# Kernel optimization log

Hardware: AMD Instinct MI355X
Metric: run time of the kernel (lower is better)

The kernel has to match this reference:

```python
import jax, jax.numpy as jnp
import numpy as np

EMBED_DIM = 1024
NUM_HEADS = 16
HEAD_DIM = EMBED_DIM // NUM_HEADS
SCALING = HEAD_DIM ** -0.5
NEG_FILL = -1e30


def setup_inputs() -> dict:
    key = jax.random.key(0)
    k1, k2, k3 = jax.random.split(key, 3)
    T, B, E = 2048, 4, EMBED_DIM
    query = jax.random.normal(k1, (T, B, E), dtype=jnp.float32)
    key_padding_mask = jnp.zeros((B, T), dtype=bool)  # 1 = padded key
    # xavier_uniform-like init
    lim_in = (6.0 / (3 * E + E)) ** 0.5
    in_proj_weight = jax.random.uniform(k2, (3 * E, E), minval=-lim_in, maxval=lim_in, dtype=jnp.float32)
    in_proj_bias = jnp.zeros((3 * E,), dtype=jnp.float32)
    lim_out = (6.0 / (E + E)) ** 0.5
    out_w = jax.random.uniform(k3, (E, E), minval=-lim_out, maxval=lim_out, dtype=jnp.float32)
    out_b = jnp.zeros((E,), dtype=jnp.float32)
    return {"query": query, "key_padding_mask": key_padding_mask,
            "in_proj_weight": in_proj_weight, "in_proj_bias": in_proj_bias,
            "out_w": out_w, "out_b": out_b}


def reference(query, key_padding_mask, in_proj_weight, in_proj_bias, out_w, out_b):
    T, B, E = query.shape
    H, D = NUM_HEADS, HEAD_DIM
    # fused in-projection (self-attention: qkv from same input)
    qkv = query @ in_proj_weight.T + in_proj_bias  # [T,B,3E]
    q, k, v = jnp.split(qkv, 3, axis=-1)
    q = q * SCALING
    q = q.reshape(T, B, H, D)
    k = k.reshape(T, B, H, D)
    v = v.reshape(T, B, H, D)
    # attention scores [B,H,T,S]
    scores = jnp.einsum('tbhd,sbhd->bhts', q, k)
    scores = jnp.where(key_padding_mask[:, None, None, :], NEG_FILL, scores)
    attn_w = jax.nn.softmax(scores, axis=-1)  # [B,H,T,S]
    # weighted sum of values -> [T,B,E]
    attn = jnp.einsum('bhts,sbhd->tbhd', attn_w, v).reshape(T, B, E)
    attn = attn @ out_w.T + out_b
    attn_w_avg = jnp.sum(attn_w, axis=1) / H  # [B,T,S]
    return attn, attn_w_avg
```

## Files before the change

### kernel.cpp

```cpp
#include <hip/hip_runtime.h>
#include <stdint.h>

#define QSCALE 0.18033688011112042f

typedef unsigned short u16;
typedef unsigned int u32;
typedef unsigned long long u64;
typedef _Float16 f16;
typedef __attribute__((ext_vector_type(2))) __fp16 h16x2;
typedef __attribute__((ext_vector_type(8))) _Float16 f16x8;
typedef __attribute__((ext_vector_type(8))) __bf16 bf16x8;
typedef __attribute__((ext_vector_type(4))) float f32x4;
typedef __attribute__((ext_vector_type(16))) float f32x16;
typedef __attribute__((ext_vector_type(8))) u16 u16x8;
typedef __attribute__((ext_vector_type(4))) u32 u32x4;

__device__ __forceinline__ void gl_lds16(const void* g, void* l) {
  __builtin_amdgcn_global_load_lds(
      (const __attribute__((address_space(1))) void*)g,
      (__attribute__((address_space(3))) void*)l, 16, 0, 0);
}

__device__ __forceinline__ u16 f2bf(float f) {
  unsigned int u = __float_as_uint(f);
  u += 0x7FFFu + ((u >> 16) & 1u);
  return (u16)(u >> 16);
}

extern "C" __global__ __launch_bounds__(256) void cvt_all(
    const float* __restrict__ query, const float* __restrict__ w_in,
    const float* __restrict__ w_out, u16* __restrict__ dst,
    const unsigned char* __restrict__ mask, u64* __restrict__ mbits) {
  if (blockIdx.x == 12288) {
    const int i = threadIdx.x;
    if (i < 128) {
      const unsigned char* p = mask + i * 64;
      u64 bits = 0;
#pragma unroll
      for (int j = 0; j < 8; ++j) {
        const u64 c = *(const u64*)(p + j * 8);
#pragma unroll
        for (int bb = 0; bb < 8; ++bb)
          if ((c >> (8 * bb)) & 0xFFull) bits |= 1ull << (j * 8 + bb);
      }
      mbits[i] = bits;
    }
    return;
  }
  int i = (blockIdx.x * 256 + threadIdx.x) * 4;
  const float* src;
  int off;
  if (i < 8388608) {
    src = query; off = i;
  } else if (i < 11534336) {
    src = w_in; off = i - 8388608;
  } else {
    src = w_out; off = i - 11534336;
  }
  float4 v = *(const float4*)(src + off);
  ushort4 o;
  o.x = f2bf(v.x); o.y = f2bf(v.y); o.z = f2bf(v.z); o.w = f2bf(v.w);
  *(ushort4*)(dst + i) = o;
}

extern "C" __global__ __launch_bounds__(256) void gemm_qkv(
    const u16* __restrict__ X, const u16* __restrict__ W,
    const float* __restrict__ bias,
    u16* __restrict__ qb, u16* __restrict__ kb, u16* __restrict__ vtb) {
  const int tid = threadIdx.x;
  const int w = tid >> 6, lane = tid & 63;
  const int lg = lane >> 4, ll = lane & 15;
  const int wm = w >> 1, wn = w & 1;

  const int xcd = blockIdx.x & 7;
  const int i6 = blockIdx.x >> 3;
  const int tx = xcd * 8 + (i6 & 7);
  const int ty = i6 >> 3;
  const int row0A = tx * 128;
  const int row0B = ty * 128;

  __shared__ __align__(16) u16 SM[16384];
  u16* Asb = SM;
  u16* Bsb = SM + 8192;

  f32x4 acc[4][4] = {};

  const int r_st = tid >> 2;
  const int cb_st = (tid & 3) * 16;

#pragma unroll
  for (int it = 0; it < 2; ++it) {
    gl_lds16((const char*)X + ((size_t)(row0A + it * 64 + r_st) * 1024) * 2 + cb_st,
             (char*)Asb + it * 4096 + w * 1024);
    gl_lds16((const char*)W + ((size_t)(row0B + it * 64 + r_st) * 1024) * 2 + cb_st,
             (char*)Bsb + it * 4096 + w * 1024);
  }

  for (int kt = 0; kt < 32; ++kt) {
    const int cur = kt & 1;
    asm volatile("s_waitcnt vmcnt(0)" ::: "memory");
    __syncthreads();
    if (kt + 1 < 32) {
      const int k0 = (kt + 1) * 32;
      const int nxt = cur ^ 1;
#pragma unroll
      for (int it = 0; it < 2; ++it) {
        gl_lds16((const char*)X + ((size_t)(row0A + it * 64 + r_st) * 1024 + k0) * 2 + cb_st,
                 (char*)(Asb + nxt * 4096) + it * 4096 + w * 1024);
        gl_lds16((const char*)W + ((size_t)(row0B + it * 64 + r_st) * 1024 + k0) * 2 + cb_st,
                 (char*)(Bsb + nxt * 4096) + it * 4096 + w * 1024);
      }
    }
    const u16* Ab = Asb + cur * 4096;
    const u16* Bb = Bsb + cur * 4096;
    const int kc = lg * 8;
    bf16x8 a[4], bfr[4];
#pragma unroll
    for (int i = 0; i < 4; ++i)
      a[i] = *(const bf16x8*)(Ab + (wm * 64 + i * 16 + ll) * 32 + kc);
#pragma unroll
    for (int j = 0; j < 4; ++j)
      bfr[j] = *(const bf16x8*)(Bb + (wn * 64 + j * 16 + ll) * 32 + kc);
#pragma unroll
    for (int i = 0; i < 4; ++i)
#pragma unroll
      for (int j = 0; j < 4; ++j)
        acc[i][j] = __builtin_amdgcn_mfma_f32_16x16x32_bf16(a[i], bfr[j], acc[i][j], 0, 0, 0);
  }

  __syncthreads();
  const int which = row0B >> 10;
  const float scl = which == 0 ? QSCALE : 1.0f;
  const int hh0 = (row0B & 1023) >> 6;

#pragma unroll
  for (int j = 0; j < 4; ++j) {
    const int n = row0B + wn * 64 + j * 16 + ll;
    const float bv = bias[n];
#pragma unroll
    for (int i = 0; i < 4; ++i)
#pragma unroll
      for (int r = 0; r < 4; ++r) {
        const float val = (acc[i][j][r] + bv) * scl;
        u16 pay;
        if (which == 2) {
          const f16 hv = (f16)val;
          pay = __builtin_bit_cast(u16, hv);
        } else {
          pay = f2bf(val);
        }
        const int lrow = wn * 128 + r * 32 + wm * 16 + i * 4 + lg;
        const int slot = (j * 2 + (ll >> 3)) ^ (lrow & 7);
        SM[lrow * 64 + slot * 8 + (ll & 7)] = pay;
      }
  }
  __syncthreads();

  if (which < 2) {
    u16* dst = which ? kb : qb;
    const int lrow = tid;
    const int hh = hh0 + (lrow >> 7);
    const int bb = (lrow >> 5) & 3;
    const int tt = (row0A >> 2) + (lrow & 31);
    u16* gp = dst + ((size_t)(bb * 16 + hh) * 2048 + tt) * 64;
#pragma unroll
    for (int s = 0; s < 8; ++s)
      *(u16x8*)(gp + s * 8) = *(const u16x8*)(SM + lrow * 64 + ((s ^ (lrow & 7)) << 3));
  } else {
#pragma unroll
    for (int u = 0; u < 2; ++u) {
      const int rid = u * 256 + tid;
      const int bb = rid >> 7, hhr = (rid >> 6) & 1, dd = rid & 63;
      const int hh = hh0 + hhr;
      const int slot0 = dd >> 3, de = dd & 7;
      u16 col[32];
#pragma unroll
      for (int t2 = 0; t2 < 32; ++t2) {
        const int lrow = hhr * 128 + bb * 32 + t2;
        col[t2] = SM[lrow * 64 + ((slot0 ^ (lrow & 7)) << 3) + de];
      }
      u16* gp = vtb + ((size_t)(bb * 16 + hh) * 64 + dd) * 2048 + (row0A >> 2);
#pragma unroll
      for (int sg = 0; sg < 4; ++sg)
        *(u16x8*)(gp + sg * 8) = *(const u16x8*)(col + sg * 8);
    }
  }
}

extern "C" __global__ __launch_bounds__(256, 4) void flash_fwd(
    const u16* __restrict__ q, const u16* __restrict__ k,
    const u16* __restrict__ vt, const u64* __restrict__ mbits,
    u16* __restrict__ attn_pre, float* __restrict__ stat_il) {
  const int lb = ((blockIdx.x & 7) << 7) + (blockIdx.x >> 3);
  const int bh = lb >> 4, tt = lb & 15;
  const int b = bh >> 4, hd = bh & 15;
  const int t0 = tt * 128;
  const int tid = threadIdx.x, w = tid >> 6, lane = tid & 63;
  const int hl = lane >> 5;
  const int l31 = lane & 31;

  __shared__ __align__(16) u16 Ks[2][64 * 64];
  __shared__ __align__(16) u16 Vs[2][64 * 64];

  const int qrow = t0 + w * 32 + l31;
  const u16* qp = q + ((size_t)bh * 2048 + qrow) * 64 + hl * 8;
  bf16x8 qreg[4];
#pragma unroll
  for (int kg = 0; kg < 4; ++kg) qreg[kg] = *(const bf16x8*)(qp + kg * 16);

  f32x16 po[2] = {};
  float ls0 = 0.f, ls1 = 0.f;
  const h16x2 ones = {(__fp16)1.0f, (__fp16)1.0f};

  const int slot_r = tid >> 3;
  const int slot_c8 = (tid & 7) ^ (slot_r & 7);

#define STAGE_F(buf, s0_)                                                      \
  do {                                                                         \
    _Pragma("unroll") for (int it2 = 0; it2 < 2; ++it2) {                      \
      const int rr = it2 * 32 + slot_r;                                        \
      gl_lds16((const char*)k +                                                \
                   (((size_t)bh * 2048 + (s0_) + rr) * 64 + slot_c8 * 8) * 2,  \
               (char*)&Ks[buf][0] + it2 * 4096 + w * 1024);                    \
      gl_lds16((const char*)vt +                                               \
                   (((size_t)bh * 64 + rr) * 2048 + (s0_) + slot_c8 * 8) * 2,  \
               (char*)&Vs[buf][0] + it2 * 4096 + w * 1024);                    \
    }                                                                          \
  } while (0)

  STAGE_F(0, 0);
  asm volatile("s_waitcnt vmcnt(0)" ::: "memory");
  __builtin_amdgcn_s_barrier();

  for (int t = 0; t < 32; ++t) {
    const u64 mb = mbits[b * 32 + t];
    const int cur = t & 1;
    if (t + 1 < 32) STAGE_F(cur ^ 1, (t + 1) * 64);

    const char* Kb = (const char*)&Ks[cur][0];
    const char* Vb = (const char*)&Vs[cur][0];

#pragma unroll
    for (int kt = 0; kt < 2; ++kt) {
      f32x16 z = {};
      const int key = kt * 32 + l31;
      __builtin_amdgcn_s_setprio(1);
#pragma unroll
      for (int kg = 0; kg < 4; ++kg) {
        const bf16x8 kf = *(const bf16x8*)(
            Kb + key * 128 + ((((kg << 1) | hl) ^ (key & 7)) << 4));
        z = __builtin_amdgcn_mfma_f32_32x32x16_bf16(kf, qreg[kg], z, 0, 0, 0);
      }
      __builtin_amdgcn_s_setprio(0);

      float ps[16];
#pragma unroll
      for (int r = 0; r < 16; ++r) ps[r] = __builtin_amdgcn_exp2f(z[r]);
      const u32 m32 = (u32)(mb >> (kt * 32));
      if (m32) {
#pragma unroll
        for (int r = 0; r < 16; ++r) {
          const int bitpos = (r & 3) + 8 * (r >> 2) + 4 * hl;
          if ((m32 >> bitpos) & 1u) ps[r] = 0.f;
        }
      }

      u32 w8[8];
#pragma unroll
      for (int j = 0; j < 8; ++j) {
        const h16x2 pk = __builtin_amdgcn_cvt_pkrtz(ps[2 * j], ps[2 * j + 1]);
        w8[j] = __builtin_bit_cast(u32, pk);
        if (j & 1)
          ls1 = __builtin_amdgcn_fdot2(pk, ones, ls1, false);
        else
          ls0 = __builtin_amdgcn_fdot2(pk, ones, ls0, false);
      }

#pragma unroll
      for (int f = 0; f < 2; ++f) {
        u32 d0 = w8[4 * f], d1 = w8[4 * f + 1];
        u32 s0w = w8[4 * f + 2], s1w = w8[4 * f + 3];
        asm volatile("v_permlane32_swap_b32 %0, %1" : "+v"(d0), "+v"(s0w));
        asm volatile("v_permlane32_swap_b32 %0, %1" : "+v"(d1), "+v"(s1w));
        const f16x8 pa = __builtin_bit_cast(f16x8, (u32x4){d0, d1, s0w, s1w});
        const int g = kt * 2 + f;
        __builtin_amdgcn_s_setprio(1);
#pragma unroll
        for (int dt = 0; dt < 2; ++dt) {
          const int d = dt * 32 + l31;
          const f16x8 vf = *(const f16x8*)(
              Vb + d * 128 + ((((g << 1) | hl) ^ (d & 7)) << 4));
          po[dt] = __builtin_amdgcn_mfma_f32_32x32x16_f16(pa, vf, po[dt], 0, 0, 0);
        }
        __builtin_amdgcn_s_setprio(0);
      }
    }

    asm volatile("s_waitcnt vmcnt(0)" ::: "memory");
    __builtin_amdgcn_s_barrier();
  }

  float lsum = ls0 + ls1;
  lsum += __shfl_xor(lsum, 32, 64);
  const float linv = 1.0f / lsum;
  if (lane < 32)
    stat_il[(size_t)bh * 2048 + t0 + w * 32 + lane] = linv;

#pragma unroll
  for (int r = 0; r < 16; ++r) {
    const int qi = (r & 3) + 8 * (r >> 2) + 4 * hl;
    const float lv = __shfl(linv, qi, 64);
    const int trow = t0 + w * 32 + qi;
#pragma unroll
    for (int dt = 0; dt < 2; ++dt) {
      const int dd = dt * 32 + l31;
      attn_pre[((size_t)(trow * 4 + b)) * 1024 + hd * 64 + dd] =
          f2bf(po[dt][r] * lv);
    }
  }
#undef STAGE_F
}

extern "C" __global__ __launch_bounds__(256, 3) void tail_fused(
    const u16* __restrict__ q, const u16* __restrict__ k,
    const u64* __restrict__ mbits, const float* __restrict__ stat_il,
    float* __restrict__ wout,
    const u16* __restrict__ A, const u16* __restrict__ Wo,
    const float* __restrict__ bias, float* __restrict__ out) {
  __shared__ __align__(16) u16 POOL[24576];
  const int bid = blockIdx.x;
  const int g5 = bid / 5, r5 = bid % 5;
  const int tid = threadIdx.x, w = tid >> 6, lane = tid & 63;

  if (r5 == 4) {
    const int lg = lane >> 4, ll = lane & 15;
    const int wm = w >> 1, wn = w & 1;
    const int xcd = g5 & 7;
    const int i6 = g5 >> 3;
    const int row0A = (xcd * 8 + (i6 & 7)) * 128;
    const int row0B = (i6 >> 3) * 128;

    u16* Asb = POOL;
    u16* Bsb = POOL + 8192;

    f32x4 acc[4][4] = {};
    const int r_st = tid >> 2;
    const int cb_st = (tid & 3) * 16;

#pragma unroll
    for (int it = 0; it < 2; ++it) {
      gl_lds16((const char*)A + ((size_t)(row0A + it * 64 + r_st) * 1024) * 2 + cb_st,
               (char*)Asb + it * 4096 + w * 1024);
      gl_lds16((const char*)Wo + ((size_t)(row0B + it * 64 + r_st) * 1024) * 2 + cb_st,
               (char*)Bsb + it * 4096 + w * 1024);
    }

    for (int kt = 0; kt < 32; ++kt) {
      const int cur = kt & 1;
      asm volatile("s_waitcnt vmcnt(0)" ::: "memory");
      __syncthreads();
      if (kt + 1 < 32) {
        const int k0 = (kt + 1) * 32;
        const int nxt = cur ^ 1;
#pragma unroll
        for (int it = 0; it < 2; ++it) {
          gl_lds16((const char*)A + ((size_t)(row0A + it * 64 + r_st) * 1024 + k0) * 2 + cb_st,
                   (char*)(Asb + nxt * 4096) + it * 4096 + w * 1024);
          gl_lds16((const char*)Wo + ((size_t)(row0B + it * 64 + r_st) * 1024 + k0) * 2 + cb_st,
                   (char*)(Bsb + nxt * 4096) + it * 4096 + w * 1024);
        }
      }
      const u16* Ab = Asb + cur * 4096;
      const u16* Bb = Bsb + cur * 4096;
      const int kc = lg * 8;
      bf16x8 a[4], bfr[4];
#pragma unroll
      for (int i = 0; i < 4; ++i)
        a[i] = *(const bf16x8*)(Ab + (wm * 64 + i * 16 + ll) * 32 + kc);
#pragma unroll
      for (int j = 0; j < 4; ++j)
        bfr[j] = *(const bf16x8*)(Bb + (wn * 64 + j * 16 + ll) * 32 + kc);
#pragma unroll
      for (int i = 0; i < 4; ++i)
#pragma unroll
        for (int j = 0; j < 4; ++j)
          acc[i][j] = __builtin_amdgcn_mfma_f32_16x16x32_bf16(a[i], bfr[j], acc[i][j], 0, 0, 0);
    }

#pragma unroll
    for (int j = 0; j < 4; ++j) {
      const int n = row0B + wn * 64 + j * 16 + ll;
      const float bv = bias[n];
#pragma unroll
      for (int i = 0; i < 4; ++i)
#pragma unroll
        for (int r = 0; r < 4; ++r) {
          const int m = row0A + wm * 64 + i * 16 + lg * 4 + r;
          out[(size_t)m * 1024 + n] = acc[i][j][r] + bv;
        }
    }
    return;
  }

  const int wb = g5 * 4 + r5;
  const int lb = ((wb & 7) << 8) + (wb >> 3);
  const int b = lb >> 9, tt = (lb >> 5) & 15, st = lb & 31;
  const int t0 = tt * 128, s0 = st * 64;
  const int hl = lane >> 5;
  const int l31 = lane & 31;

  const int slot_r8 = tid >> 3;
  const int slot_c8 = (tid & 7) ^ (slot_r8 & 7);

  const u64 mbw = mbits[b * 32 + st];
  const u32 m32lo = (u32)mbw, m32hi = (u32)(mbw >> 32);
  const bool domask = mbw != 0ull;

#define STAGE_W(buf, hh)                                                       \
  do {                                                                         \
    const size_t qo_ = (size_t)(b * 16 + (hh)) * 2048;                         \
    _Pragma("unroll") for (int i2 = 0; i2 < 4; ++i2) {                         \
      const int rr = i2 * 32 + slot_r8;                                        \
      gl_lds16((const char*)q + ((qo_ + t0 + rr) * 64 + slot_c8 * 8) * 2,      \
               (char*)(POOL + (buf)*8192) + i2 * 4096 + w * 1024);             \
    }                                                                          \
    _Pragma("unroll") for (int i2 = 0; i2 < 2; ++i2) {                         \
      const int rr = i2 * 32 + slot_r8;                                        \
      gl_lds16((const char*)k + ((qo_ + s0 + rr) * 64 + slot_c8 * 8) * 2,      \
               (char*)(POOL + 16384 + (buf)*4096) + i2 * 4096 + w * 1024);     \
    }                                                                          \
  } while (0)

  STAGE_W(0, 0);
  asm volatile("s_waitcnt vmcnt(0)" ::: "memory");
  __syncthreads();

  float accw[32] = {};
  for (int h = 0; h < 16; ++h) {
    const int cur = h & 1;
    const float ilh =
        stat_il[(size_t)(b * 16 + h) * 2048 + t0 + w * 32 + l31];

    if (h + 1 < 16) STAGE_W(cur ^ 1, h + 1);

    const char* Qb = (const char*)(POOL + cur * 8192);
    const char* Kb = (const char*)(POOL + 16384 + cur * 4096);

    const int qr = w * 32 + l31;
    bf16x8 qf[4];
#pragma unroll
    for (int kg = 0; kg < 4; ++kg)
      qf[kg] = *(const bf16x8*)(
          Qb + qr * 128 + ((((kg << 1) | hl) ^ (qr & 7)) << 4));

    f32x16 z0 = {}, z1 = {};
    __builtin_amdgcn_s_setprio(1);
#pragma unroll
    for (int kg = 0; kg < 4; ++kg) {
      const int key = l31;
      const bf16x8 kf = *(const bf16x8*)(
          Kb + key * 128 + ((((kg << 1) | hl) ^ (key & 7)) << 4));
      z0 = __builtin_amdgcn_mfma_f32_32x32x16_bf16(kf, qf[kg], z0, 0, 0, 0);
    }
#pragma unroll
    for (int kg = 0; kg < 4; ++kg) {
      const int key = 32 + l31;
      const bf16x8 kf = *(const bf16x8*)(
          Kb + key * 128 + ((((kg << 1) | hl) ^ (key & 7)) << 4));
      z1 = __builtin_amdgcn_mfma_f32_32x32x16_bf16(kf, qf[kg], z1, 0, 0, 0);
    }
    __builtin_amdgcn_s_setprio(0);

#pragma unroll
    for (int r = 0; r < 16; ++r) {
      float p = __builtin_amdgcn_exp2f(z0[r]);
      if (domask) {
        const int bitpos = (r & 3) + 8 * (r >> 2) + 4 * hl;
        if ((m32lo >> bitpos) & 1u) p = 0.f;
      }
      accw[r] = fmaf(p, ilh, accw[r]);
    }
#pragma unroll
    for (int r = 0; r < 16; ++r) {
      float p = __builtin_amdgcn_exp2f(z1[r]);
      if (domask) {
        const int bitpos = (r & 3) + 8 * (r >> 2) + 4 * hl;
        if ((m32hi >> bitpos) & 1u) p = 0.f;
      }
      accw[16 + r] = fmaf(p, ilh, accw[16 + r]);
    }

    asm volatile("s_waitcnt vmcnt(0)" ::: "memory");
    __syncthreads();
  }

  float* tb = ((float*)POOL) + w * 2048;
#pragma unroll
  for (int kt = 0; kt < 2; ++kt)
#pragma unroll
    for (int j = 0; j < 4; ++j) {
      f32x4 qd;
#pragma unroll
      for (int e = 0; e < 4; ++e) qd[e] = accw[kt * 16 + 4 * j + e] * 0.0625f;
      const int slot = kt * 8 + 2 * j + hl;
      *(f32x4*)(tb + l31 * 64 + ((slot ^ (l31 & 7)) << 2)) = qd;
    }
  __syncthreads();
#pragma unroll
  for (int j2 = 0; j2 < 8; ++j2) {
    const int row = j2 * 4 + (lane >> 4);
    const int slot = lane & 15;
    const f32x4 v = *(const f32x4*)(tb + row * 64 + ((slot ^ (row & 7)) << 2));
    *(f32x4*)(wout + ((size_t)b * 2048 + t0 + w * 32 + row) * 2048 + s0 +
              slot * 4) = v;
  }
#undef STAGE_W
}

extern "C" void kernel_launch(void* const* d_in, const int* in_sizes, int n_in,
                              void* d_out, int out_size, void* d_ws, size_t ws_size,
                              hipStream_t stream) {
  const float* query = (const float*)d_in[0];
  const unsigned char* mask = (const unsigned char*)d_in[1];
  const float* w_in = (const float*)d_in[2];
  const float* b_in = (const float*)d_in[3];
  const float* w_out = (const float*)d_in[4];
  const float* b_out = (const float*)d_in[5];

  float* out0 = (float*)d_out;
  float* outw = out0 + (size_t)8388608;

  char* ws = (char*)d_ws;
  u16* Xbf   = (u16*)(ws + 0);
  u16* Wqkv  = (u16*)(ws + 16777216);
  u16* Woutb = (u16*)(ws + 23068672);
  u16* qb    = (u16*)(ws + 25165824);
  u16* kb    = (u16*)(ws + 41943040);
  u16* vtb   = (u16*)(ws + 75497472);
  u16* ap    = (u16*)(ws + 92274688);
  float* sil = (float*)(ws + 109051904);
  u64* mbits = (u64*)(ws + 109576192);

  cvt_all<<<12289, 256, 0, stream>>>(query, w_in, w_out, Xbf, mask, mbits);
  gemm_qkv<<<1536, 256, 0, stream>>>(Xbf, Wqkv, b_in, qb, kb, vtb);
  flash_fwd<<<1024, 256, 0, stream>>>(qb, kb, vtb, mbits, ap, sil);
  tail_fused<<<2560, 256, 0, stream>>>(qb, kb, mbits, sil, outw,
                                       ap, Woutb, b_out, out0);
}
```

Baseline: 269.5 us.

## Widen attention-weight tiles to 128 keys per block in tail kernel

The tail kernel's attention-weight blocks now cover 128 key columns instead of 64, so each Q tile staged per head is reused across twice as many keys. That halves Q loads and block count. The grid shrinks from 2560 to 1536 blocks, still interleaving one out-projection GEMM block for every two weight blocks. LDS grows to 64 KB and the accumulator doubles to 64 floats, so occupancy is lowered to 2 blocks per SM. The output write-back is rewritten so each thread stores half of a 128-wide row.

```diff
diff --git a/kernel.cpp b/kernel.cpp
--- a/kernel.cpp
+++ b/kernel.cpp
@@ -321,22 +321,22 @@
 #undef STAGE_F
 }
 
-extern "C" __global__ __launch_bounds__(256, 3) void tail_fused(
+extern "C" __global__ __launch_bounds__(256, 2) void tail_fused(
     const u16* __restrict__ q, const u16* __restrict__ k,
     const u64* __restrict__ mbits, const float* __restrict__ stat_il,
     float* __restrict__ wout,
     const u16* __restrict__ A, const u16* __restrict__ Wo,
     const float* __restrict__ bias, float* __restrict__ out) {
-  __shared__ __align__(16) u16 POOL[24576];
+  __shared__ __align__(16) u16 POOL[32768];
   const int bid = blockIdx.x;
-  const int g5 = bid / 5, r5 = bid % 5;
+  const int g3 = bid / 3, r3 = bid % 3;
   const int tid = threadIdx.x, w = tid >> 6, lane = tid & 63;
 
-  if (r5 == 4) {
+  if (r3 == 2) {
     const int lg = lane >> 4, ll = lane & 15;
     const int wm = w >> 1, wn = w & 1;
-    const int xcd = g5 & 7;
-    const int i6 = g5 >> 3;
+    const int xcd = g3 & 7;
+    const int i6 = g3 >> 3;
     const int row0A = (xcd * 8 + (i6 & 7)) * 128;
     const int row0B = (i6 >> 3) * 128;
 
@@ -402,19 +402,24 @@
     return;
   }
 
-  const int wb = g5 * 4 + r5;
-  const int lb = ((wb & 7) << 8) + (wb >> 3);
-  const int b = lb >> 9, tt = (lb >> 5) & 15, st = lb & 31;
-  const int t0 = tt * 128, s0 = st * 64;
+  const int wb = g3 * 2 + r3;
+  const int lb = ((wb & 7) << 7) + (wb >> 3);
+  const int b = lb >> 8, tt = (lb >> 4) & 15, sp = lb & 15;
+  const int t0 = tt * 128, s0 = sp * 128;
   const int hl = lane >> 5;
   const int l31 = lane & 31;
 
   const int slot_r8 = tid >> 3;
   const int slot_c8 = (tid & 7) ^ (slot_r8 & 7);
 
-  const u64 mbw = mbits[b * 32 + st];
-  const u32 m32lo = (u32)mbw, m32hi = (u32)(mbw >> 32);
-  const bool domask = mbw != 0ull;
+  u32 m32t[4];
+  {
+    const u64 mb0 = mbits[b * 32 + sp * 2];
+    const u64 mb1 = mbits[b * 32 + sp * 2 + 1];
+    m32t[0] = (u32)mb0; m32t[1] = (u32)(mb0 >> 32);
+    m32t[2] = (u32)mb1; m32t[3] = (u32)(mb1 >> 32);
+  }
+  const bool domask = (m32t[0] | m32t[1] | m32t[2] | m32t[3]) != 0u;
 
 #define STAGE_W(buf, hh)                                                       \
   do {                                                                         \
@@ -423,11 +428,8 @@
       const int rr = i2 * 32 + slot_r8;                                        \
       gl_lds16((const char*)q + ((qo_ + t0 + rr) * 64 + slot_c8 * 8) * 2,      \
                (char*)(POOL + (buf)*8192) + i2 * 4096 + w * 1024);             \
-    }                                                                          \
-    _Pragma("unroll") for (int i2 = 0; i2 < 2; ++i2) {                         \
-      const int rr = i2 * 32 + slot_r8;                                        \
       gl_lds16((const char*)k + ((qo_ + s0 + rr) * 64 + slot_c8 * 8) * 2,      \
-               (char*)(POOL + 16384 + (buf)*4096) + i2 * 4096 + w * 1024);     \
+               (char*)(POOL + 16384 + (buf)*8192) + i2 * 4096 + w * 1024);     \
     }                                                                          \
   } while (0)
 
@@ -435,7 +437,7 @@
   asm volatile("s_waitcnt vmcnt(0)" ::: "memory");
   __syncthreads();
 
-  float accw[32] = {};
+  float accw[64] = {};
   for (int h = 0; h < 16; ++h) {
     const int cur = h & 1;
     const float ilh =
@@ -444,7 +446,7 @@
     if (h + 1 < 16) STAGE_W(cur ^ 1, h + 1);
 
     const char* Qb = (const char*)(POOL + cur * 8192);
-    const char* Kb = (const char*)(POOL + 16384 + cur * 4096);
+    const char* Kb = (const char*)(POOL + 16384 + cur * 8192);
 
     const int qr = w * 32 + l31;
     bf16x8 qf[4];
@@ -453,66 +455,55 @@
       qf[kg] = *(const bf16x8*)(
           Qb + qr * 128 + ((((kg << 1) | hl) ^ (qr & 7)) << 4));
 
-    f32x16 z0 = {}, z1 = {};
-    __builtin_amdgcn_s_setprio(1);
-#pragma unroll
-    for (int kg = 0; kg < 4; ++kg) {
-      const int key = l31;
-      const bf16x8 kf = *(const bf16x8*)(
-          Kb + key * 128 + ((((kg << 1) | hl) ^ (key & 7)) << 4));
-      z0 = __builtin_amdgcn_mfma_f32_32x32x16_bf16(kf, qf[kg], z0, 0, 0, 0);
-    }
-#pragma unroll
-    for (int kg = 0; kg < 4; ++kg) {
-      const int key = 32 + l31;
-      const bf16x8 kf = *(const bf16x8*)(
-          Kb + key * 128 + ((((kg << 1) | hl) ^ (key & 7)) << 4));
-      z1 = __builtin_amdgcn_mfma_f32_32x32x16_bf16(kf, qf[kg], z1, 0, 0, 0);
-    }
-    __builtin_amdgcn_s_setprio(0);
-
-#pragma unroll
-    for (int r = 0; r < 16; ++r) {
-      float p = __builtin_amdgcn_exp2f(z0[r]);
-      if (domask) {
-        const int bitpos = (r & 3) + 8 * (r >> 2) + 4 * hl;
-        if ((m32lo >> bitpos) & 1u) p = 0.f;
-      }
-      accw[r] = fmaf(p, ilh, accw[r]);
-    }
-#pragma unroll
-    for (int r = 0; r < 16; ++r) {
-      float p = __builtin_amdgcn_exp2f(z1[r]);
-      if (domask) {
-        const int bitpos = (r & 3) + 8 * (r >> 2) + 4 * hl;
-        if ((m32hi >> bitpos) & 1u) p = 0.f;
-      }
-      accw[16 + r] = fmaf(p, ilh, accw[16 + r]);
+#pragma unroll
+    for (int kt = 0; kt < 4; ++kt) {
+      f32x16 z = {};
+      const int key = kt * 32 + l31;
+      __builtin_amdgcn_s_setprio(1);
+#pragma unroll
+      for (int kg = 0; kg < 4; ++kg) {
+        const bf16x8 kf = *(const bf16x8*)(
+            Kb + key * 128 + ((((kg << 1) | hl) ^ (key & 7)) << 4));
+        z = __builtin_amdgcn_mfma_f32_32x32x16_bf16(kf, qf[kg], z, 0, 0, 0);
+      }
+      __builtin_amdgcn_s_setprio(0);
+#pragma unroll
+      for (int r = 0; r < 16; ++r) {
+        float p = __builtin_amdgcn_exp2f(z[r]);
+        if (domask) {
+          const int bitpos = (r & 3) + 8 * (r >> 2) + 4 * hl;
+          if ((m32t[kt] >> bitpos) & 1u) p = 0.f;
+        }
+        accw[kt * 16 + r] = fmaf(p, ilh, accw[kt * 16 + r]);
+      }
     }
 
     asm volatile("s_waitcnt vmcnt(0)" ::: "memory");
     __syncthreads();
   }
 
-  float* tb = ((float*)POOL) + w * 2048;
-#pragma unroll
-  for (int kt = 0; kt < 2; ++kt)
-#pragma unroll
-    for (int j = 0; j < 4; ++j) {
+  float* tb = (float*)POOL;
+#pragma unroll
+  for (int kt = 0; kt < 4; ++kt)
+#pragma unroll
+    for (int q8 = 0; q8 < 4; ++q8) {
       f32x4 qd;
 #pragma unroll
-      for (int e = 0; e < 4; ++e) qd[e] = accw[kt * 16 + 4 * j + e] * 0.0625f;
-      const int slot = kt * 8 + 2 * j + hl;
-      *(f32x4*)(tb + l31 * 64 + ((slot ^ (l31 & 7)) << 2)) = qd;
+      for (int e = 0; e < 4; ++e) qd[e] = accw[kt * 16 + q8 * 4 + e] * 0.0625f;
+      const int row = w * 32 + l31;
+      const int slot = kt * 8 + q8 * 2 + hl;
+      *(f32x4*)(tb + row * 128 + ((slot ^ (row & 7)) << 2)) = qd;
     }
   __syncthreads();
-#pragma unroll
-  for (int j2 = 0; j2 < 8; ++j2) {
-    const int row = j2 * 4 + (lane >> 4);
-    const int slot = lane & 15;
-    const f32x4 v = *(const f32x4*)(tb + row * 64 + ((slot ^ (row & 7)) << 2));
-    *(f32x4*)(wout + ((size_t)b * 2048 + t0 + w * 32 + row) * 2048 + s0 +
-              slot * 4) = v;
+  {
+    const int row = tid >> 1, h2 = tid & 1;
+    float* gbase = wout + ((size_t)b * 2048 + t0 + row) * 2048 + s0;
+#pragma unroll
+    for (int u = 0; u < 16; ++u) {
+      const int slot = h2 * 16 + u;
+      const f32x4 v = *(const f32x4*)(tb + row * 128 + ((slot ^ (row & 7)) << 2));
+      *(f32x4*)(gbase + slot * 4) = v;
+    }
   }
 #undef STAGE_W
 }
@@ -544,6 +535,6 @@
   cvt_all<<<12289, 256, 0, stream>>>(query, w_in, w_out, Xbf, mask, mbits);
   gemm_qkv<<<1536, 256, 0, stream>>>(Xbf, Wqkv, b_in, qb, kb, vtb);
   flash_fwd<<<1024, 256, 0, stream>>>(qb, kb, vtb, mbits, ap, sil);
-  tail_fused<<<2560, 256, 0, stream>>>(qb, kb, mbits, sil, outw,
+  tail_fused<<<1536, 256, 0, stream>>>(qb, kb, mbits, sil, outw,
                                        ap, Woutb, b_out, out0);
 }
```

Result: slower. 293.8 us (+9.0%).
